# Optimization experiments

Measured on AMD Instinct MI355X. Metric: run time of the kernel, lower is better.

## Reference

```python
import jax, jax.numpy as jnp
import numpy as np

EPS = 1e-6

def wave_repr(x, global_mode):
    # x: [B,S,D]
    x = jnp.clip(x, -10.0, 10.0)
    xsq = x * x
    if global_mode:
        Gsq = jnp.sum(xsq, axis=(1, 2), keepdims=True) + EPS  # [B,1,1]
    else:
        Gsq = jnp.sum(xsq, axis=1, keepdims=True) + EPS       # [B,1,D]
    G = jnp.maximum(jnp.sqrt(Gsq), EPS)
    # NOTE: source uses torch.div(..., rounding_mode='floor') -> floor division
    ratio = jnp.clip(jnp.floor(x / G), -0.99, 0.99)
    sqrt_term = jnp.sqrt(jnp.maximum(1.0 - ratio * ratio, EPS))
    alpha = jnp.arctan2(sqrt_term, ratio)
    return G * jnp.cos(alpha), G * jnp.sin(alpha)

def gelu(x):
    return jax.nn.gelu(x, approximate=False)

def rmsnorm(x, w):
    return x * jax.lax.rsqrt(jnp.mean(x * x, axis=-1, keepdims=True) + EPS) * w

def setup_inputs() -> dict:
    key = jax.random.key(0)
    B, S, D = 4, 4096, 1024
    ks = jax.random.split(key, 16)
    s = 0.02
    p = {
        'x': jax.random.normal(ks[0], (B, S, D), jnp.float32),
        'Wa': jax.random.normal(ks[1], (D, D)) * s, 'ba': jnp.zeros((D,)),
        'Wp': jax.random.normal(ks[2], (D, D)) * s, 'bp': jnp.zeros((D,)),
        'gate_bias': jnp.zeros((D,)),
        'w1r': jax.random.normal(ks[3], (D, 4 * D)) * s, 'b1r': jnp.zeros((4 * D,)),
        'w2r': jax.random.normal(ks[4], (4 * D, D)) * s, 'b2r': jnp.zeros((D,)),
        'w1i': jax.random.normal(ks[5], (D, 4 * D)) * s, 'b1i': jnp.zeros((4 * D,)),
        'w2i': jax.random.normal(ks[6], (4 * D, D)) * s, 'b2i': jnp.zeros((D,)),
        'We': jax.random.normal(ks[7], (2 * D, D)) * s, 'be': jnp.zeros((D,)),
        'g_rms': jnp.ones((D,)),
        'wf1': jax.random.normal(ks[8], (D, 2 * D)) * s, 'bf1': jnp.zeros((2 * D,)),
        'wf2': jax.random.normal(ks[9], (2 * D, D)) * s, 'bf2': jnp.zeros((D,)),
    }
    return p

def reference(x, Wa, ba, Wp, bp, gate_bias, w1r, b1r, w2r, b2r, w1i, b1i, w2i, b2i, We, be, g_rms, wf1, bf1, wf2, bf2):
    # wave representations: global (sentence) + local (token)
    rs, is_ = wave_repr(x, True)
    rt, it = wave_repr(x, False)
    cr = rs + rt
    ci = is_ + it
    # amplitude / phase
    amp = jnp.sqrt(cr * cr + ci * ci + EPS)
    ph = jnp.arctan2(ci, cr)
    # biological noise gate (eval mode: no noise)
    gate = jax.nn.sigmoid(amp @ Wa + ba + ph @ Wp + bp + gate_bias)
    gr = cr * gate
    gi = ci * gate
    rp = gelu(gr @ w1r + b1r) @ w2r + b2r
    ip = gelu(gi @ w1i + b1i) @ w2i + b2i
    # combine to embedding + RMSNorm
    wave = jnp.concatenate([rp, ip], axis=-1) @ We + be
    out = rmsnorm(wave, g_rms)
    y = gelu(out @ wf1 + bf1) @ wf2 + bf2
    return y
```

## Files before the change

### kernel.cpp

```cpp
#include <hip/hip_runtime.h>
#include <cmath>

typedef _Float16 f16;
typedef _Float16 f16x8 __attribute__((ext_vector_type(8)));
typedef _Float16 f16x4 __attribute__((ext_vector_type(4)));
typedef float f32x4 __attribute__((ext_vector_type(4)));

#define EPSF 1e-6f

__device__ __forceinline__ void gload16(const f16* g, const f16* l) {
  __builtin_amdgcn_global_load_lds(
      (__attribute__((address_space(1))) void*)g,
      (__attribute__((address_space(3))) void*)l, 16, 0, 0);
}

__device__ __forceinline__ float fast_gelu(float u) {
  const float z = u * 0.70710678118654752f;
  const float az = fabsf(z);
  const float t = __builtin_amdgcn_rcpf(fmaf(0.3275911f, az, 1.0f));
  float p = 1.061405429f;
  p = fmaf(p, t, -1.453152027f);
  p = fmaf(p, t, 1.421413741f);
  p = fmaf(p, t, -0.284496736f);
  p = fmaf(p, t, 0.254829592f);
  p = p * t;
  const float e = __expf(-az * az);
  float er = fmaf(-p, e, 1.0f);
  er = copysignf(er, z);
  return 0.5f * u * (1.0f + er);
}

__global__ void wtr_k(const float* __restrict__ W, f16* __restrict__ WT, int K, int N) {
  __shared__ float t[32][33];
  const int nb = blockIdx.x * 32, kb = blockIdx.y * 32;
  const int tx = threadIdx.x, ty = threadIdx.y;
#pragma unroll
  for (int i = ty; i < 32; i += 8) t[i][tx] = W[(size_t)(kb + i) * N + nb + tx];
  __syncthreads();
#pragma unroll
  for (int i = ty; i < 32; i += 8) WT[(size_t)(nb + i) * K + kb + tx] = (f16)t[tx][i];
}

__global__ void cast_k(const float* __restrict__ W, f16* __restrict__ H) {
  const size_t i = (size_t)blockIdx.x * 256 + threadIdx.x;
  const float4 v = ((const float4*)W)[i];
  f16x4 o;
  o[0] = (f16)v.x; o[1] = (f16)v.y; o[2] = (f16)v.z; o[3] = (f16)v.w;
  ((f16x4*)H)[i] = o;
}

__global__ void colsq_k(const float* __restrict__ x, float* __restrict__ part) {
  const int d = blockIdx.x * 256 + threadIdx.x;
  const int sb = blockIdx.y;
  const int b = blockIdx.z;
  const float* p = x + ((size_t)b * 4096 + (size_t)sb * 256) * 1024 + d;
  float acc = 0.f;
#pragma unroll 4
  for (int s = 0; s < 256; ++s) {
    float v = p[(size_t)s * 1024];
    v = fminf(fmaxf(v, -10.f), 10.f);
    acc = fmaf(v, v, acc);
  }
  part[((size_t)b * 16 + sb) * 1024 + d] = acc;
}

__global__ void stats_k(const float* __restrict__ part, float* __restrict__ Gsum,
                        float* __restrict__ amp) {
  const int b = blockIdx.x;
  const int t = threadIdx.x;
  __shared__ double red[256];
  float cs[4];
  double tot = 0.0;
#pragma unroll
  for (int i = 0; i < 4; ++i) {
    const int d = t + i * 256;
    double s = 0.0;
    for (int k = 0; k < 16; ++k) s += (double)part[((size_t)b * 16 + k) * 1024 + d];
    cs[i] = (float)s;
    tot += s;
  }
  red[t] = tot;
  __syncthreads();
  for (int st = 128; st > 0; st >>= 1) {
    if (t < st) red[t] += red[t + st];
    __syncthreads();
  }
  const float Gs = fmaxf(sqrtf((float)red[0] + EPSF), EPSF);
#pragma unroll
  for (int i = 0; i < 4; ++i) {
    const int d = t + i * 256;
    const float Gt = fmaxf(sqrtf(cs[i] + EPSF), EPSF);
    const float gs = Gs + Gt;
    Gsum[(b << 10) + d] = gs;
    amp[(b << 10) + d] = sqrtf(gs * gs + EPSF);
  }
}

__global__ void rtp_k(const float* __restrict__ amp, const float* __restrict__ Wa,
                      double* __restrict__ part) {
  const int d = blockIdx.x * 256 + threadIdx.x;
  const int b = blockIdx.y;
  const int kc = blockIdx.z;
  const float* a = amp + (b << 10);
  double acc = 0.0;
  for (int jj = 0; jj < 128; ++jj) {
    const int k = kc * 128 + jj;
    acc += (double)a[k] * (double)Wa[((size_t)k << 10) + d];
  }
  part[(((size_t)b * 8 + kc) << 10) + d] = acc;
}
__global__ void rtr_k(const double* __restrict__ part, const float* __restrict__ ba,
                      const float* __restrict__ bp, const float* __restrict__ gbias,
                      float* __restrict__ rt) {
  const int d = blockIdx.x * 256 + threadIdx.x;
  const int b = blockIdx.y;
  double acc = 0.0;
#pragma unroll
  for (int kc = 0; kc < 8; ++kc) acc += part[(((size_t)b * 8 + kc) << 10) + d];
  rt[(b << 10) + d] = (float)acc + ba[d] + bp[d] + gbias[d];
}

__global__ void bcp_k(const float* __restrict__ b2r, const float* __restrict__ b2i,
                      const float* __restrict__ We, double* __restrict__ part) {
  const int n = blockIdx.x * 256 + threadIdx.x;
  const int kc = blockIdx.y;
  double acc = 0.0;
  for (int jj = 0; jj < 128; ++jj) {
    const int j = kc * 128 + jj;
    const float bv = (j < 1024) ? b2r[j] : b2i[j - 1024];
    acc += (double)bv * (double)We[(size_t)j * 1024 + n];
  }
  part[((size_t)kc << 10) + n] = acc;
}
__global__ void bcr_k(const double* __restrict__ part, const float* __restrict__ be,
                      float* __restrict__ bc) {
  const int n = blockIdx.x * 256 + threadIdx.x;
  double acc = 0.0;
#pragma unroll
  for (int kc = 0; kc < 16; ++kc) acc += part[((size_t)kc << 10) + n];
  bc[n] = (float)acc + be[n];
}

__global__ void ph_k(const float* __restrict__ x, f16* __restrict__ ph, float phPos,
                     float phNeg) {
  const size_t i = (size_t)blockIdx.x * 256 + threadIdx.x;
  const float4 v = ((const float4*)x)[i];
  f16x4 o;
  o[0] = (f16)(v.x < 0.f ? phNeg : phPos);
  o[1] = (f16)(v.y < 0.f ? phNeg : phPos);
  o[2] = (f16)(v.z < 0.f ? phNeg : phPos);
  o[3] = (f16)(v.w < 0.f ? phNeg : phPos);
  ((f16x4*)ph)[i] = o;
}

__global__ void rms_k(const float* __restrict__ wave, const float* __restrict__ g,
                      f16* __restrict__ o) {
  const size_t row = blockIdx.x;
  const int t = threadIdx.x;
  const float4 v = ((const float4*)(wave + row * 1024))[t];
  float ss = v.x * v.x + v.y * v.y + v.z * v.z + v.w * v.w;
#pragma unroll
  for (int s = 32; s > 0; s >>= 1) ss += __shfl_down(ss, s);
  __shared__ float red[4];
  if ((t & 63) == 0) red[t >> 6] = ss;
  __syncthreads();
  const float tot = red[0] + red[1] + red[2] + red[3];
  const float r = rsqrtf(tot * (1.f / 1024.f) + EPSF);
  const float4 gv = ((const float4*)g)[t];
  f16x4 ov;
  ov[0] = (f16)(v.x * r * gv.x);
  ov[1] = (f16)(v.y * r * gv.y);
  ov[2] = (f16)(v.z * r * gv.z);
  ov[3] = (f16)(v.w * r * gv.w);
  ((f16x4*)(o + row * 1024))[t] = ov;
}

template <int EPI>
__global__ __launch_bounds__(512, 4) void gemm2_k(
    const f16* __restrict__ A, int lda, const f16* __restrict__ BT, int ldb, int K,
    const float* __restrict__ bias, f16* __restrict__ outH, int ldo) {
  __shared__ __align__(16) char smem[49152];
  f16(*smA)[4096] = reinterpret_cast<f16(*)[4096]>(smem);
  f16(*smB)[8192] = reinterpret_cast<f16(*)[8192]>(smem + 16384);
  const int tid = threadIdx.x;
  const int w = tid >> 6, l = tid & 63;

  const int ncol = gridDim.y;
  const int bid = blockIdx.x * ncol + blockIdx.y;
  const int nwg = gridDim.x * ncol;
  const int q = nwg >> 3, rr = nwg & 7;
  const int xcd = bid & 7, idx = bid >> 3;
  const int swz = (xcd < rr ? xcd * (q + 1) : rr * (q + 1) + (xcd - rr) * q) + idx;
  const int bx = swz / ncol, by = swz % ncol;
  const size_t rbase = (size_t)bx * 128;
  const size_t cbase = (size_t)by * 256;

  const int srow = (w << 4) + (l >> 2);
  const int slot = l & 3;
  const int ss = ((slot ^ ((srow >> 1) & 3)) << 3);

  f32x4 acc[4][4];
  const f32x4 zero = {0.f, 0.f, 0.f, 0.f};
#pragma unroll
  for (int m = 0; m < 4; ++m)
#pragma unroll
    for (int n = 0; n < 4; ++n) acc[m][n] = zero;

  const f16* gA = A + (rbase + srow) * (size_t)lda + ss;
  const f16* gB0 = BT + (cbase + srow) * (size_t)ldb + ss;
  const f16* gB1 = BT + (cbase + srow + 128) * (size_t)ldb + ss;

  const int nk = K >> 5;
  auto stage = [&](int buf, size_t ko) {
    gload16(gA + ko, &smA[buf][w << 9]);
    gload16(gB0 + ko, &smB[buf][w << 9]);
    gload16(gB1 + ko, &smB[buf][4096 + (w << 9)]);
  };
  stage(0, 0);
  __syncthreads();

  const int arow = l & 15;
  const int kg = (((l >> 4) ^ ((arow >> 1) & 3)) << 3);
  const int wr = (w >> 2) << 6;
  const int wc = (w & 3) << 6;

  for (int t = 0; t < nk; ++t) {
    const int cur = t & 1;
    if (t + 1 < nk) stage(cur ^ 1, (size_t)(t + 1) << 5);
    const f16* ap = &smA[cur][(wr + arow) * 32 + kg];
    const f16* bp = &smB[cur][(wc + arow) * 32 + kg];
    f16x8 af[4], bf[4];
#pragma unroll
    for (int m = 0; m < 4; ++m) af[m] = *(const f16x8*)(ap + m * 512);
#pragma unroll
    for (int n = 0; n < 4; ++n) bf[n] = *(const f16x8*)(bp + n * 512);
#pragma unroll
    for (int m = 0; m < 4; ++m)
#pragma unroll
      for (int n = 0; n < 4; ++n)
        acc[m][n] = __builtin_amdgcn_mfma_f32_16x16x32_f16(af[m], bf[n], acc[m][n], 0, 0, 0);
    __syncthreads();
  }

  const int fr = l & 15, hi = l >> 4;
  const int r4 = hi << 2;
  float* ep = reinterpret_cast<float*>(smem + w * 4352);
#pragma unroll
  for (int m = 0; m < 4; ++m) {
#pragma unroll
    for (int n = 0; n < 4; ++n) {
      const int cl = n * 16 + fr;
#pragma unroll
      for (int j = 0; j < 4; ++j) {
        float v = acc[m][n][j];
        if constexpr (EPI == 3) v = fast_gelu(v + bias[cbase + wc + cl]);
        ep[(r4 + j) * 68 + cl] = v;
      }
    }
    asm volatile("s_waitcnt lgkmcnt(0)" ::: "memory");
    __builtin_amdgcn_sched_barrier(0);
#pragma unroll
    for (int it = 0; it < 2; ++it) {
      const int rl = l >> 2;
      const int ch = (l & 3) + it * 4;
      const float* pr = &ep[rl * 68 + ch * 8];
      f16x8 o;
#pragma unroll
      for (int e = 0; e < 8; ++e) o[e] = (f16)pr[e];
      *(f16x8*)&outH[(rbase + wr + m * 16 + rl) * (size_t)ldo + (cbase + wc + ch * 8)] = o;
    }
    asm volatile("s_waitcnt lgkmcnt(0)" ::: "memory");
    __builtin_amdgcn_sched_barrier(0);
  }
}

template <int EPI>
__global__ __launch_bounds__(256, 5) void gemm1_k(
    const f16* __restrict__ A, int lda, const f16* __restrict__ BT, int ldb, int K,
    const float* __restrict__ bias, float* __restrict__ outF, int ldo,
    const f16* __restrict__ phm, const float* __restrict__ rowterm,
    const float* __restrict__ Gsum, f16* __restrict__ gr, f16* __restrict__ gi, int r0,
    float ratioNeg, float stNeg) {
  __shared__ __align__(16) char smem[32768];
  f16(*smA)[4096] = reinterpret_cast<f16(*)[4096]>(smem);
  f16(*smB)[4096] = reinterpret_cast<f16(*)[4096]>(smem + 16384);
  const int tid = threadIdx.x;
  const int wv = tid >> 6, ln = tid & 63;

  const int ncol = gridDim.y;
  const int bid = blockIdx.x * ncol + blockIdx.y;
  const int nwg = gridDim.x * ncol;
  const int q = nwg >> 3, rr = nwg & 7;
  const int xcd = bid & 7, idx = bid >> 3;
  const int swz = (xcd < rr ? xcd * (q + 1) : rr * (q + 1) + (xcd - rr) * q) + idx;
  const int bx = swz / ncol, by = swz % ncol;
  const size_t rbase = (size_t)bx * 128;
  const size_t cbase = (size_t)by * 128;

  const int srow = (wv << 4) + (ln >> 2);
  const int slot = ln & 3;
  const int ss = ((slot ^ ((srow >> 1) & 3)) << 3);

  f32x4 acc[4][4];
  const f32x4 zero = {0.f, 0.f, 0.f, 0.f};
#pragma unroll
  for (int m = 0; m < 4; ++m)
#pragma unroll
    for (int n = 0; n < 4; ++n) acc[m][n] = zero;

  const f16* gA = A + (rbase + srow) * (size_t)lda + ss;
  const f16* gB = BT + (cbase + srow) * (size_t)ldb + ss;

  const int nk = K >> 5;
  auto stage = [&](int buf, size_t ko) {
    gload16(gA + ko, &smA[buf][wv << 9]);
    gload16(gA + ko + (size_t)64 * lda, &smA[buf][2048 + (wv << 9)]);
    gload16(gB + ko, &smB[buf][wv << 9]);
    gload16(gB + ko + (size_t)64 * ldb, &smB[buf][2048 + (wv << 9)]);
  };
  stage(0, 0);
  __syncthreads();

  const int arow = ln & 15;
  const int kg = (((ln >> 4) ^ ((arow >> 1) & 3)) << 3);
  const int wr = (wv >> 1) << 6;
  const int wc = (wv & 1) << 6;

  for (int t = 0; t < nk; ++t) {
    const int cur = t & 1;
    if (t + 1 < nk) stage(cur ^ 1, (size_t)(t + 1) << 5);
    const f16* ap = &smA[cur][(wr + arow) * 32 + kg];
    const f16* bp = &smB[cur][(wc + arow) * 32 + kg];
    f16x8 af[4], bf[4];
#pragma unroll
    for (int m = 0; m < 4; ++m) af[m] = *(const f16x8*)(ap + m * 512);
#pragma unroll
    for (int n = 0; n < 4; ++n) bf[n] = *(const f16x8*)(bp + n * 512);
#pragma unroll
    for (int m = 0; m < 4; ++m)
#pragma unroll
      for (int n = 0; n < 4; ++n)
        acc[m][n] = __builtin_amdgcn_mfma_f32_16x16x32_f16(af[m], bf[n], acc[m][n], 0, 0, 0);
    __syncthreads();
  }

  const int fr = ln & 15, hi = ln >> 4;
  const int r4 = hi << 2;

  if constexpr (EPI == 4) {
    float* ep = reinterpret_cast<float*>(smem + wv * 4352);
#pragma unroll
    for (int m = 0; m < 4; ++m) {
      float grv[4][4], giv[4][4];
#pragma unroll
      for (int n = 0; n < 4; ++n) {
        const size_t col = cbase + wc + n * 16 + fr;
#pragma unroll
        for (int j = 0; j < 4; ++j) {
          const size_t row = rbase + wr + m * 16 + r4 + j;
          const int gb = (int)(((size_t)r0 + row) >> 12);
          const float pre = acc[m][n][j] + rowterm[((size_t)gb << 10) + col];
          const float gate = __builtin_amdgcn_rcpf(1.f + __expf(-pre));
          const float ph = (float)phm[row * 1024 + col];
          const bool neg = ph > 2.f;
          const float gs = Gsum[((size_t)gb << 10) + col];
          grv[n][j] = (neg ? gs * ratioNeg : 0.f) * gate;
          giv[n][j] = gs * (neg ? stNeg : 1.f) * gate;
        }
      }
#pragma unroll
      for (int pass = 0; pass < 2; ++pass) {
        f16* dst = pass ? gi : gr;
#pragma unroll
        for (int n = 0; n < 4; ++n)
#pragma unroll
          for (int j = 0; j < 4; ++j)
            ep[(r4 + j) * 68 + n * 16 + fr] = pass ? giv[n][j] : grv[n][j];
        asm volatile("s_waitcnt lgkmcnt(0)" ::: "memory");
        __builtin_amdgcn_sched_barrier(0);
#pragma unroll
        for (int it = 0; it < 2; ++it) {
          const int rl = ln >> 2;
          const int ch = (ln & 3) + it * 4;
          const float* pr = &ep[rl * 68 + ch * 8];
          f16x8 o;
#pragma unroll
          for (int e = 0; e < 8; ++e) o[e] = (f16)pr[e];
          *(f16x8*)&dst[(rbase + wr + m * 16 + rl) * 1024 + (cbase + wc + ch * 8)] = o;
        }
        asm volatile("s_waitcnt lgkmcnt(0)" ::: "memory");
        __builtin_amdgcn_sched_barrier(0);
      }
    }
  } else {
#pragma unroll
    for (int m = 0; m < 4; ++m) {
#pragma unroll
      for (int n = 0; n < 4; ++n) {
        const size_t col = cbase + wc + n * 16 + fr;
#pragma unroll
        for (int j = 0; j < 4; ++j) {
          const size_t row = rbase + wr + m * 16 + r4 + j;
          const float v = acc[m][n][j];
          if constexpr (EPI == 0) {
            outF[row * (size_t)ldo + col] = v + bias[col];
          } else {
            outF[row * (size_t)ldo + col] += v;
          }
        }
      }
    }
  }
}

extern "C" void kernel_launch(void* const* d_in, const int* in_sizes, int n_in,
                              void* d_out, int out_size, void* d_ws, size_t ws_size,
                              hipStream_t stream) {
  const float* x     = (const float*)d_in[0];
  const float* Wa    = (const float*)d_in[1];
  const float* ba    = (const float*)d_in[2];
  const float* Wp    = (const float*)d_in[3];
  const float* bp    = (const float*)d_in[4];
  const float* gbias = (const float*)d_in[5];
  const float* w1r   = (const float*)d_in[6];
  const float* b1r   = (const float*)d_in[7];
  const float* w2r   = (const float*)d_in[8];
  const float* b2r   = (const float*)d_in[9];
  const float* w1i   = (const float*)d_in[10];
  const float* b1i   = (const float*)d_in[11];
  const float* w2i   = (const float*)d_in[12];
  const float* b2i   = (const float*)d_in[13];
  const float* We    = (const float*)d_in[14];
  const float* be    = (const float*)d_in[15];
  const float* grms  = (const float*)d_in[16];
  const float* wf1   = (const float*)d_in[17];
  const float* bf1   = (const float*)d_in[18];
  const float* wf2   = (const float*)d_in[19];
  const float* bf2   = (const float*)d_in[20];
  float* out = (float*)d_out;

  char* ws = (char*)d_ws;
  size_t off = 0;
  auto alloc = [&](size_t bytes) -> void* {
    void* p = (void*)(ws + off);
    off += (bytes + 255) & ~(size_t)255;
    return p;
  };

  f16* WpT   = (f16*)alloc((size_t)1024 * 1024 * 2);
  f16* w1rT  = (f16*)alloc((size_t)4096 * 1024 * 2);
  f16* w1iT  = (f16*)alloc((size_t)4096 * 1024 * 2);
  f16* wf1T  = (f16*)alloc((size_t)2048 * 1024 * 2);
  f16* wf2T  = (f16*)alloc((size_t)1024 * 2048 * 2);
  f16* WcrT  = (f16*)alloc((size_t)1024 * 4096 * 2);
  f16* WciT  = (f16*)alloc((size_t)1024 * 4096 * 2);
  float* part    = (float*)alloc((size_t)4 * 16 * 1024 * 4);
  float* GsumB   = (float*)alloc((size_t)4 * 1024 * 4);
  float* ampB    = (float*)alloc((size_t)4 * 1024 * 4);
  float* rowterm = (float*)alloc((size_t)4 * 1024 * 4);
  float* bcB     = (float*)alloc((size_t)1024 * 4);
  double* rtPart = (double*)alloc((size_t)4 * 8 * 1024 * 8);
  double* bcPart = (double*)alloc((size_t)16 * 1024 * 8);
  const size_t staticEnd = off;

  char* tmp = ws + staticEnd;
  f16* WeT  = (f16*)tmp;
  f16* w2rH = (f16*)(tmp + (size_t)4 * 1024 * 1024);
  f16* w2iH = (f16*)(tmp + (size_t)12 * 1024 * 1024);

  {
    dim3 b(32, 8);
    wtr_k<<<dim3(32, 32), b, 0, stream>>>(Wp, WpT, 1024, 1024);
    wtr_k<<<dim3(128, 32), b, 0, stream>>>(w1r, w1rT, 1024, 4096);
    wtr_k<<<dim3(128, 32), b, 0, stream>>>(w1i, w1iT, 1024, 4096);
    wtr_k<<<dim3(64, 32), b, 0, stream>>>(wf1, wf1T, 1024, 2048);
    wtr_k<<<dim3(32, 64), b, 0, stream>>>(wf2, wf2T, 2048, 1024);
    wtr_k<<<dim3(32, 64), b, 0, stream>>>(We, WeT, 2048, 1024);
    cast_k<<<dim3(4096), 256, 0, stream>>>(w2r, w2rH);
    cast_k<<<dim3(4096), 256, 0, stream>>>(w2i, w2iH);
  }

  colsq_k<<<dim3(4, 16, 4), 256, 0, stream>>>(x, part);
  stats_k<<<4, 256, 0, stream>>>(part, GsumB, ampB);
  rtp_k<<<dim3(4, 4, 8), 256, 0, stream>>>(ampB, Wa, rtPart);
  rtr_k<<<dim3(4, 4), 256, 0, stream>>>(rtPart, ba, bp, gbias, rowterm);
  bcp_k<<<dim3(4, 16), 256, 0, stream>>>(b2r, b2i, We, bcPart);
  bcr_k<<<dim3(4), 256, 0, stream>>>(bcPart, be, bcB);

  gemm2_k<5><<<dim3(8, 16), 512, 0, stream>>>(WeT, 2048, w2rH, 1024, 1024, nullptr,
      WcrT, 4096);
  gemm2_k<5><<<dim3(8, 16), 512, 0, stream>>>(WeT + 1024, 2048, w2iH, 1024, 1024, nullptr,
      WciT, 4096);

  const float ratioNeg = -0.99f;
  const float stNeg = sqrtf(fmaxf(1.0f - 0.99f * 0.99f, EPSF));
  const float phPos = atan2f(1.0f, 0.0f);
  const float phNeg = atan2f(stNeg, ratioNeg);

  const long Ntok = (long)in_sizes[0] / 1024;
  const size_t perRow = 14336;
  long R = (long)((ws_size > staticEnd ? ws_size - staticEnd : 0) / perRow);
  R &= ~255L;
  if (R > 8192) R = 8192;
  if (R < 256) R = 256;

  char* cb = ws + staticEnd;
  f16* phB = (f16*)cb;
  f16* grB = (f16*)(cb + (size_t)R * 2048);
  f16* giB = (f16*)(cb + (size_t)R * 4096);
  f16* h1B = (f16*)(cb + (size_t)R * 6144);
  float* waveF = (float*)phB;
  f16* outB = giB;
  f16* h2B = h1B;

  for (long r0 = 0; r0 < Ntok; r0 += R) {
    const long Rc = (Ntok - r0 < R) ? (Ntok - r0) : R;
    const int gm = (int)(Rc / 128);
    ph_k<<<dim3((int)Rc), 256, 0, stream>>>(x + r0 * 1024, phB, phPos, phNeg);
    gemm1_k<4><<<dim3(gm, 8), 256, 0, stream>>>(phB, 1024, WpT, 1024, 1024, nullptr,
        nullptr, 1024, phB, rowterm, GsumB, grB, giB, (int)r0, ratioNeg, stNeg);
    gemm2_k<3><<<dim3(gm, 16), 512, 0, stream>>>(grB, 1024, w1rT, 1024, 1024, b1r,
        h1B, 4096);
    gemm1_k<0><<<dim3(gm, 8), 256, 0, stream>>>(h1B, 4096, WcrT, 4096, 4096, bcB,
        waveF, 1024, nullptr, nullptr, nullptr, nullptr, nullptr, 0, 0.f, 0.f);
    gemm2_k<3><<<dim3(gm, 16), 512, 0, stream>>>(giB, 1024, w1iT, 1024, 1024, b1i,
        h1B, 4096);
    gemm1_k<1><<<dim3(gm, 8), 256, 0, stream>>>(h1B, 4096, WciT, 4096, 4096, nullptr,
        waveF, 1024, nullptr, nullptr, nullptr, nullptr, nullptr, 0, 0.f, 0.f);
    rms_k<<<dim3((int)Rc), 256, 0, stream>>>(waveF, grms, outB);
    gemm2_k<3><<<dim3(gm, 8), 512, 0, stream>>>(outB, 1024, wf1T, 1024, 1024, bf1,
        h2B, 2048);
    gemm1_k<0><<<dim3(gm, 8), 256, 0, stream>>>(h2B, 2048, wf2T, 2048, 2048, bf2,
        out + r0 * 1024, 1024, nullptr, nullptr, nullptr, nullptr, nullptr, 0, 0.f, 0.f);
  }
}
```

Before: 1.487 ms.

## Merge N=1024 GEMMs into 128x256-tile kernel and lift chunk size cap

Removes the 128x128-tile, 256-thread gemm1_k and sends all N=1024 GEMMs (gate, both down-projection/combine GEMMs, final FFN) through the 512-thread 128x256-tile gemm2_k, whose epilogue now also handles the gate and fp32-output variants. Wider tiles raise data reuse per workgroup but halve the number of workgroups for these GEMMs, which can hurt occupancy and CU fill. The row-chunk cap moves from 8192 to the full token count, so with a large enough workspace the whole batch runs in one pass with fewer launches and larger grids.

Result: faster. 1.314 ms (-11.6%).

```diff
diff --git a/kernel.cpp b/kernel.cpp
--- a/kernel.cpp
+++ b/kernel.cpp
@@ -178,7 +178,10 @@
 template <int EPI>
 __global__ __launch_bounds__(512, 4) void gemm2_k(
     const f16* __restrict__ A, int lda, const f16* __restrict__ BT, int ldb, int K,
-    const float* __restrict__ bias, f16* __restrict__ outH, int ldo) {
+    const float* __restrict__ bias, float* __restrict__ outF, f16* __restrict__ outH,
+    int ldo, const f16* __restrict__ phm, const float* __restrict__ rowterm,
+    const float* __restrict__ Gsum, f16* __restrict__ gr, f16* __restrict__ gi, int r0,
+    float ratioNeg, float stNeg) {
   __shared__ __align__(16) char smem[49152];
   f16(*smA)[4096] = reinterpret_cast<f16(*)[4096]>(smem);
   f16(*smB)[8192] = reinterpret_cast<f16(*)[8192]>(smem + 16384);
@@ -244,111 +247,38 @@
 
   const int fr = l & 15, hi = l >> 4;
   const int r4 = hi << 2;
-  float* ep = reinterpret_cast<float*>(smem + w * 4352);
-#pragma unroll
-  for (int m = 0; m < 4; ++m) {
-#pragma unroll
-    for (int n = 0; n < 4; ++n) {
-      const int cl = n * 16 + fr;
-#pragma unroll
-      for (int j = 0; j < 4; ++j) {
-        float v = acc[m][n][j];
-        if constexpr (EPI == 3) v = fast_gelu(v + bias[cbase + wc + cl]);
-        ep[(r4 + j) * 68 + cl] = v;
+
+  if constexpr (EPI == 3 || EPI == 5) {
+    float* ep = reinterpret_cast<float*>(smem + w * 4352);
+#pragma unroll
+    for (int m = 0; m < 4; ++m) {
+#pragma unroll
+      for (int n = 0; n < 4; ++n) {
+        const int cl = n * 16 + fr;
+#pragma unroll
+        for (int j = 0; j < 4; ++j) {
+          float v = acc[m][n][j];
+          if constexpr (EPI == 3) v = fast_gelu(v + bias[cbase + wc + cl]);
+          ep[(r4 + j) * 68 + cl] = v;
+        }
       }
+      asm volatile("s_waitcnt lgkmcnt(0)" ::: "memory");
+      __builtin_amdgcn_sched_barrier(0);
+#pragma unroll
+      for (int it = 0; it < 2; ++it) {
+        const int rl = l >> 2;
+        const int ch = (l & 3) + it * 4;
+        const float* pr = &ep[rl * 68 + ch * 8];
+        f16x8 o;
+#pragma unroll
+        for (int e = 0; e < 8; ++e) o[e] = (f16)pr[e];
+        *(f16x8*)&outH[(rbase + wr + m * 16 + rl) * (size_t)ldo + (cbase + wc + ch * 8)] = o;
+      }
+      asm volatile("s_waitcnt lgkmcnt(0)" ::: "memory");
+      __builtin_amdgcn_sched_barrier(0);
     }
-    asm volatile("s_waitcnt lgkmcnt(0)" ::: "memory");
-    __builtin_amdgcn_sched_barrier(0);
-#pragma unroll
-    for (int it = 0; it < 2; ++it) {
-      const int rl = l >> 2;
-      const int ch = (l & 3) + it * 4;
-      const float* pr = &ep[rl * 68 + ch * 8];
-      f16x8 o;
-#pragma unroll
-      for (int e = 0; e < 8; ++e) o[e] = (f16)pr[e];
-      *(f16x8*)&outH[(rbase + wr + m * 16 + rl) * (size_t)ldo + (cbase + wc + ch * 8)] = o;
-    }
-    asm volatile("s_waitcnt lgkmcnt(0)" ::: "memory");
-    __builtin_amdgcn_sched_barrier(0);
-  }
-}
-
-template <int EPI>
-__global__ __launch_bounds__(256, 5) void gemm1_k(
-    const f16* __restrict__ A, int lda, const f16* __restrict__ BT, int ldb, int K,
-    const float* __restrict__ bias, float* __restrict__ outF, int ldo,
-    const f16* __restrict__ phm, const float* __restrict__ rowterm,
-    const float* __restrict__ Gsum, f16* __restrict__ gr, f16* __restrict__ gi, int r0,
-    float ratioNeg, float stNeg) {
-  __shared__ __align__(16) char smem[32768];
-  f16(*smA)[4096] = reinterpret_cast<f16(*)[4096]>(smem);
-  f16(*smB)[4096] = reinterpret_cast<f16(*)[4096]>(smem + 16384);
-  const int tid = threadIdx.x;
-  const int wv = tid >> 6, ln = tid & 63;
-
-  const int ncol = gridDim.y;
-  const int bid = blockIdx.x * ncol + blockIdx.y;
-  const int nwg = gridDim.x * ncol;
-  const int q = nwg >> 3, rr = nwg & 7;
-  const int xcd = bid & 7, idx = bid >> 3;
-  const int swz = (xcd < rr ? xcd * (q + 1) : rr * (q + 1) + (xcd - rr) * q) + idx;
-  const int bx = swz / ncol, by = swz % ncol;
-  const size_t rbase = (size_t)bx * 128;
-  const size_t cbase = (size_t)by * 128;
-
-  const int srow = (wv << 4) + (ln >> 2);
-  const int slot = ln & 3;
-  const int ss = ((slot ^ ((srow >> 1) & 3)) << 3);
-
-  f32x4 acc[4][4];
-  const f32x4 zero = {0.f, 0.f, 0.f, 0.f};
-#pragma unroll
-  for (int m = 0; m < 4; ++m)
-#pragma unroll
-    for (int n = 0; n < 4; ++n) acc[m][n] = zero;
-
-  const f16* gA = A + (rbase + srow) * (size_t)lda + ss;
-  const f16* gB = BT + (cbase + srow) * (size_t)ldb + ss;
-
-  const int nk = K >> 5;
-  auto stage = [&](int buf, size_t ko) {
-    gload16(gA + ko, &smA[buf][wv << 9]);
-    gload16(gA + ko + (size_t)64 * lda, &smA[buf][2048 + (wv << 9)]);
-    gload16(gB + ko, &smB[buf][wv << 9]);
-    gload16(gB + ko + (size_t)64 * ldb, &smB[buf][2048 + (wv << 9)]);
-  };
-  stage(0, 0);
-  __syncthreads();
-
-  const int arow = ln & 15;
-  const int kg = (((ln >> 4) ^ ((arow >> 1) & 3)) << 3);
-  const int wr = (wv >> 1) << 6;
-  const int wc = (wv & 1) << 6;
-
-  for (int t = 0; t < nk; ++t) {
-    const int cur = t & 1;
-    if (t + 1 < nk) stage(cur ^ 1, (size_t)(t + 1) << 5);
-    const f16* ap = &smA[cur][(wr + arow) * 32 + kg];
-    const f16* bp = &smB[cur][(wc + arow) * 32 + kg];
-    f16x8 af[4], bf[4];
-#pragma unroll
-    for (int m = 0; m < 4; ++m) af[m] = *(const f16x8*)(ap + m * 512);
-#pragma unroll
-    for (int n = 0; n < 4; ++n) bf[n] = *(const f16x8*)(bp + n * 512);
-#pragma unroll
-    for (int m = 0; m < 4; ++m)
-#pragma unroll
-      for (int n = 0; n < 4; ++n)
-        acc[m][n] = __builtin_amdgcn_mfma_f32_16x16x32_f16(af[m], bf[n], acc[m][n], 0, 0, 0);
-    __syncthreads();
-  }
-
-  const int fr = ln & 15, hi = ln >> 4;
-  const int r4 = hi << 2;
-
-  if constexpr (EPI == 4) {
-    float* ep = reinterpret_cast<float*>(smem + wv * 4352);
+  } else if constexpr (EPI == 4) {
+    float* ep = reinterpret_cast<float*>(smem + w * 4352);
 #pragma unroll
     for (int m = 0; m < 4; ++m) {
       float grv[4][4], giv[4][4];
@@ -380,8 +310,8 @@
         __builtin_amdgcn_sched_barrier(0);
 #pragma unroll
         for (int it = 0; it < 2; ++it) {
-          const int rl = ln >> 2;
-          const int ch = (ln & 3) + it * 4;
+          const int rl = l >> 2;
+          const int ch = (l & 3) + it * 4;
           const float* pr = &ep[rl * 68 + ch * 8];
           f16x8 o;
 #pragma unroll
@@ -488,9 +418,9 @@
   bcr_k<<<dim3(4), 256, 0, stream>>>(bcPart, be, bcB);
 
   gemm2_k<5><<<dim3(8, 16), 512, 0, stream>>>(WeT, 2048, w2rH, 1024, 1024, nullptr,
-      WcrT, 4096);
+      nullptr, WcrT, 4096, nullptr, nullptr, nullptr, nullptr, nullptr, 0, 0.f, 0.f);
   gemm2_k<5><<<dim3(8, 16), 512, 0, stream>>>(WeT + 1024, 2048, w2iH, 1024, 1024, nullptr,
-      WciT, 4096);
+      nullptr, WciT, 4096, nullptr, nullptr, nullptr, nullptr, nullptr, 0, 0.f, 0.f);
 
   const float ratioNeg = -0.99f;
   const float stNeg = sqrtf(fmaxf(1.0f - 0.99f * 0.99f, EPSF));
@@ -501,7 +431,7 @@
   const size_t perRow = 14336;
   long R = (long)((ws_size > staticEnd ? ws_size - staticEnd : 0) / perRow);
   R &= ~255L;
-  if (R > 8192) R = 8192;
+  if (R > Ntok) R = Ntok;
   if (R < 256) R = 256;
 
   char* cb = ws + staticEnd;
@@ -517,20 +447,20 @@
     const long Rc = (Ntok - r0 < R) ? (Ntok - r0) : R;
     const int gm = (int)(Rc / 128);
     ph_k<<<dim3((int)Rc), 256, 0, stream>>>(x + r0 * 1024, phB, phPos, phNeg);
-    gemm1_k<4><<<dim3(gm, 8), 256, 0, stream>>>(phB, 1024, WpT, 1024, 1024, nullptr,
-        nullptr, 1024, phB, rowterm, GsumB, grB, giB, (int)r0, ratioNeg, stNeg);
+    gemm2_k<4><<<dim3(gm, 4), 512, 0, stream>>>(phB, 1024, WpT, 1024, 1024, nullptr,
+        nullptr, nullptr, 1024, phB, rowterm, GsumB, grB, giB, (int)r0, ratioNeg, stNeg);
     gemm2_k<3><<<dim3(gm, 16), 512, 0, stream>>>(grB, 1024, w1rT, 1024, 1024, b1r,
-        h1B, 4096);
-    gemm1_k<0><<<dim3(gm, 8), 256, 0, stream>>>(h1B, 4096, WcrT, 4096, 4096, bcB,
-        waveF, 1024, nullptr, nullptr, nullptr, nullptr, nullptr, 0, 0.f, 0.f);
+        nullptr, h1B, 4096, nullptr, nullptr, nullptr, nullptr, nullptr, 0, 0.f, 0.f);
+    gemm2_k<0><<<dim3(gm, 4), 512, 0, stream>>>(h1B, 4096, WcrT, 4096, 4096, bcB,
+        waveF, nullptr, 1024, nullptr, nullptr, nullptr, nullptr, nullptr, 0, 0.f, 0.f);
     gemm2_k<3><<<dim3(gm, 16), 512, 0, stream>>>(giB, 1024, w1iT, 1024, 1024, b1i,
-        h1B, 4096);
-    gemm1_k<1><<<dim3(gm, 8), 256, 0, stream>>>(h1B, 4096, WciT, 4096, 4096, nullptr,
-        waveF, 1024, nullptr, nullptr, nullptr, nullptr, nullptr, 0, 0.f, 0.f);
+        nullptr, h1B, 4096, nullptr, nullptr, nullptr, nullptr, nullptr, 0, 0.f, 0.f);
+    gemm2_k<1><<<dim3(gm, 4), 512, 0, stream>>>(h1B, 4096, WciT, 4096, 4096, nullptr,
+        waveF, nullptr, 1024, nullptr, nullptr, nullptr, nullptr, nullptr, 0, 0.f, 0.f);
     rms_k<<<dim3((int)Rc), 256, 0, stream>>>(waveF, grms, outB);
     gemm2_k<3><<<dim3(gm, 8), 512, 0, stream>>>(outB, 1024, wf1T, 1024, 1024, bf1,
-        h2B, 2048);
-    gemm1_k<0><<<dim3(gm, 8), 256, 0, stream>>>(h2B, 2048, wf2T, 2048, 2048, bf2,
-        out + r0 * 1024, 1024, nullptr, nullptr, nullptr, nullptr, nullptr, 0, 0.f, 0.f);
-  }
-}
+        nullptr, h2B, 2048, nullptr, nullptr, nullptr, nullptr, nullptr, 0, 0.f, 0.f);
+    gemm2_k<0><<<dim3(gm, 4), 512, 0, stream>>>(h2B, 2048, wf2T, 2048, 2048, bf2,
+        out + r0 * 1024, nullptr, 1024, nullptr, nullptr, nullptr, nullptr, nullptr, 0, 0.f, 0.f);
+  }
+}
```
